# Performance work log

Hardware: AMD Instinct MI355X
Metric: run time of the kernel (lower is better)

The kernel has to match this reference:

```python
import jax, jax.numpy as jnp
import numpy as np

N_HEADS = 16
HEAD_DIM = 128
EPS = 1e-6


def _rmsnorm(t, w):
    # RMSNorm over last dim (head_dim)
    var = jnp.mean(jnp.square(t), axis=-1, keepdims=True)
    return t * jax.lax.rsqrt(var + EPS) * w


def _apply_rope(t, freqs):
    # t: [b, s, h, d]; freqs: [s, 1, d//2, 2, 2]
    b, s, h, d = t.shape
    t2 = t.reshape(b, s, h, 2, d // 2)
    t_ = jnp.moveaxis(t2, -2, -1)[..., None, :].astype(jnp.float32)  # [b,s,h,d/2,1,2]
    out = freqs[..., 0] * t_[..., 0] + freqs[..., 1] * t_[..., 1]    # [b,s,h,d/2,2]
    out = jnp.moveaxis(out, -1, -2).reshape(b, s, h, d)
    return out.astype(t.dtype)


def setup_inputs() -> dict:
    key = jax.random.key(0)
    ks = jax.random.split(key, 8)
    B, S, D = 2, 2048, 2048
    inner = N_HEADS * HEAD_DIM
    sc = 1.0 / np.sqrt(D)
    return {
        "x": jax.random.normal(ks[0], (B, S, D), jnp.float32),
        "rope_emb": jax.random.normal(ks[1], (S, 1, HEAD_DIM // 2, 2, 2), jnp.float32),
        "Wq": jax.random.normal(ks[2], (inner, D), jnp.float32) * sc,
        "Wk": jax.random.normal(ks[3], (inner, D), jnp.float32) * sc,
        "Wv": jax.random.normal(ks[4], (inner, D), jnp.float32) * sc,
        "Wo": jax.random.normal(ks[5], (D, inner), jnp.float32) * sc,
        "q_norm_w": jnp.ones((HEAD_DIM,), jnp.float32),
        "k_norm_w": jnp.ones((HEAD_DIM,), jnp.float32),
    }


def reference(x, rope_emb, Wq, Wk, Wv, Wo, q_norm_w, k_norm_w):
    b, s, _ = x.shape
    h, d = N_HEADS, HEAD_DIM
    q = (x @ Wq.T).reshape(b, s, h, d)
    k = (x @ Wk.T).reshape(b, s, h, d)
    v = (x @ Wv.T).reshape(b, s, h, d)
    q = _apply_rope(_rmsnorm(q, q_norm_w), rope_emb)
    k = _apply_rope(_rmsnorm(k, k_norm_w), rope_emb)
    # SDPA, heads-first layout
    qh = jnp.transpose(q, (0, 2, 1, 3))  # [b,h,s,d]
    kh = jnp.transpose(k, (0, 2, 1, 3))
    vh = jnp.transpose(v, (0, 2, 1, 3))
    scale = 1.0 / np.sqrt(d)
    scores = jnp.einsum('bhqd,bhkd->bhqk', qh, kh) * scale
    attn = jax.nn.softmax(scores, axis=-1)
    out = jnp.einsum('bhqk,bhkd->bhqd', attn, vh)  # [b,h,s,d]
    out = jnp.transpose(out, (0, 2, 1, 3)).reshape(b, s, h * d)
    return out @ Wo.T
```

## Files before the change

### kernel.cpp

```cpp
#include <hip/hip_runtime.h>
#include <hip/hip_bf16.h>
#include <stdint.h>

typedef __bf16 bf16;
typedef __bf16 bf16x4 __attribute__((ext_vector_type(4)));
typedef __bf16 bf16x8 __attribute__((ext_vector_type(8)));
typedef float f32x4 __attribute__((ext_vector_type(4)));
typedef float f32x16 __attribute__((ext_vector_type(16)));

#define N_HEADS 16
#define HEAD_DIM 128
#define SEQ 2048
#define DIM 2048
#define BATCH 2
#define MROWS (BATCH * SEQ)
#define NQKV (3 * DIM)
#define SM_SCALE 0.08838834764831845f
#define SMAX 24.0f

__device__ __forceinline__ bf16 f2b(float f) {
  union { __hip_bfloat16 h; bf16 b; } u;
  u.h = __float2bfloat16(f);
  return u.b;
}

__device__ __forceinline__ void async16(const bf16* g, bf16* l) {
  __builtin_amdgcn_global_load_lds(
      (__attribute__((address_space(1))) void*)(uintptr_t)g,
      (__attribute__((address_space(3))) void*)(uintptr_t)l,
      16, 0, 0);
}

__global__ __launch_bounds__(256) void cvt_kernel(const float* __restrict__ src,
                                                  bf16* __restrict__ dst, int n) {
  int i = (blockIdx.x * 256 + threadIdx.x) * 8;
  if (i >= n) return;
  float4 a = *(const float4*)(src + i);
  float4 b = *(const float4*)(src + i + 4);
  bf16x8 o;
  o[0] = f2b(a.x); o[1] = f2b(a.y); o[2] = f2b(a.z); o[3] = f2b(a.w);
  o[4] = f2b(b.x); o[5] = f2b(b.y); o[6] = f2b(b.z); o[7] = f2b(b.w);
  *(bf16x8*)(dst + i) = o;
}

__device__ __forceinline__ void gemm_tile_mainloop(
    const bf16* __restrict__ A, const bf16* __restrict__ Bw, int K,
    int rowBase, int colBase, bf16* lA, bf16* lB, f32x4 acc[4][4]) {
  const int t = threadIdx.x;
  const int w = t >> 6, lane = t & 63;
  const int lm = lane & 15, quad = lane >> 4;
  const int wr = (w >> 1) * 64, wc = (w & 1) * 64;

  for (int kt = 0; kt < K; kt += 32) {
#pragma unroll
    for (int i = 0; i < 2; i++) {
      const int c = i * 256 + t;
      const int r = c >> 2, cc = (c & 3) << 3;
      async16(A + (size_t)(rowBase + r) * K + (kt + cc), lA + (i * 256 + w * 64) * 8);
      async16(Bw + (size_t)(colBase + r) * K + (kt + cc), lB + (i * 256 + w * 64) * 8);
    }
    asm volatile("s_waitcnt vmcnt(0)" ::: "memory");
    __syncthreads();
    bf16x8 af[4], bfr[4];
#pragma unroll
    for (int f = 0; f < 4; f++)
      af[f] = *(const bf16x8*)(lA + (wr + f * 16 + lm) * 32 + quad * 8);
#pragma unroll
    for (int f = 0; f < 4; f++)
      bfr[f] = *(const bf16x8*)(lB + (wc + f * 16 + lm) * 32 + quad * 8);
#pragma unroll
    for (int fr = 0; fr < 4; fr++)
#pragma unroll
      for (int fc = 0; fc < 4; fc++)
        acc[fr][fc] = __builtin_amdgcn_mfma_f32_16x16x32_bf16(af[fr], bfr[fc], acc[fr][fc], 0, 0, 0);
    __syncthreads();
  }
}

__global__ __launch_bounds__(256) void gemm_qkv(const bf16* __restrict__ X,
                                                const bf16* __restrict__ W,
                                                bf16* __restrict__ Q,
                                                bf16* __restrict__ Kv,
                                                bf16* __restrict__ VT) {
  __shared__ __align__(16) bf16 lA[128 * 32];
  __shared__ __align__(16) bf16 lB[128 * 32];
  f32x4 acc[4][4];
  f32x4 z = {0.f, 0.f, 0.f, 0.f};
#pragma unroll
  for (int i = 0; i < 4; i++)
#pragma unroll
    for (int j = 0; j < 4; j++) acc[i][j] = z;

  const int rowBase = blockIdx.y * 128, colBase = blockIdx.x * 128;
  gemm_tile_mainloop(X, W, DIM, rowBase, colBase, lA, lB, acc);

  const int t = threadIdx.x, w = t >> 6, lane = t & 63;
  const int lm = lane & 15, quad = lane >> 4;
  const int wr = (w >> 1) * 64, wc = (w & 1) * 64;
  const int which = colBase >> 11;
  if (which < 2) {
    bf16* dst = which ? Kv : Q;
#pragma unroll
    for (int fr = 0; fr < 4; fr++)
#pragma unroll
      for (int fc = 0; fc < 4; fc++)
#pragma unroll
        for (int r = 0; r < 4; r++) {
          int m = rowBase + wr + fr * 16 + quad * 4 + r;
          int n = (colBase + wc + fc * 16 + lm) & 2047;
          int h = n >> 7, d = n & 127;
          int b = m >> 11, s = m & 2047;
          dst[(((size_t)(b * N_HEADS + h) * SEQ) + s) * HEAD_DIM + d] = f2b(acc[fr][fc][r]);
        }
  } else {
#pragma unroll
    for (int fr = 0; fr < 4; fr++)
#pragma unroll
      for (int fc = 0; fc < 4; fc++) {
        int n = (colBase + wc + fc * 16 + lm) & 2047;
        int h = n >> 7, d = n & 127;
        int m = rowBase + wr + fr * 16 + quad * 4;
        int b = m >> 11, s = m & 2047;
        bf16x4 pk;
#pragma unroll
        for (int r = 0; r < 4; r++) pk[r] = f2b(acc[fr][fc][r]);
        *(bf16x4*)&VT[((size_t)(b * N_HEADS + h) * HEAD_DIM + d) * SEQ + s] = pk;
      }
  }
}

__global__ __launch_bounds__(256) void gemm_out(const bf16* __restrict__ A,
                                                const bf16* __restrict__ W,
                                                float* __restrict__ out) {
  __shared__ __align__(16) bf16 lA[128 * 32];
  __shared__ __align__(16) bf16 lB[128 * 32];
  f32x4 acc[4][4];
  f32x4 z = {0.f, 0.f, 0.f, 0.f};
#pragma unroll
  for (int i = 0; i < 4; i++)
#pragma unroll
    for (int j = 0; j < 4; j++) acc[i][j] = z;

  const int rowBase = blockIdx.y * 128, colBase = blockIdx.x * 128;
  gemm_tile_mainloop(A, W, DIM, rowBase, colBase, lA, lB, acc);

  const int t = threadIdx.x, w = t >> 6, lane = t & 63;
  const int lm = lane & 15, quad = lane >> 4;
  const int wr = (w >> 1) * 64, wc = (w & 1) * 64;
#pragma unroll
  for (int fr = 0; fr < 4; fr++)
#pragma unroll
    for (int fc = 0; fc < 4; fc++)
#pragma unroll
      for (int r = 0; r < 4; r++) {
        int m = rowBase + wr + fr * 16 + quad * 4 + r;
        int n = colBase + wc + fc * 16 + lm;
        out[(size_t)m * DIM + n] = acc[fr][fc][r];
      }
}

__global__ __launch_bounds__(256) void norm_rope(bf16* __restrict__ Q,
                                                 bf16* __restrict__ K,
                                                 const float* __restrict__ rope,
                                                 const float* __restrict__ qw,
                                                 const float* __restrict__ kw) {
  const int t = threadIdx.x, w = t >> 6, lane = t & 63;
  const int rid = blockIdx.x * 4 + w;
  const int which = rid >> 16;
  const int row = rid & 65535;
  bf16* ptr = (which ? K : Q) + (size_t)row * HEAD_DIM;
  const float* nw = which ? kw : qw;
  const int s = row & (SEQ - 1);

  float x0 = (float)ptr[lane];
  float x1 = (float)ptr[lane + 64];
  float ss = x0 * x0 + x1 * x1;
#pragma unroll
  for (int off = 32; off; off >>= 1) ss += __shfl_xor(ss, off);
  float r = rsqrtf(ss * (1.f / 128.f) + 1e-6f);
  float x0n = x0 * r * nw[lane];
  float x1n = x1 * r * nw[lane + 64];
  float4 f = ((const float4*)rope)[s * 64 + lane];
  float y0 = f.x * x0n + f.y * x1n;
  float y1 = f.z * x0n + f.w * x1n;
  if (!which) { y0 *= SM_SCALE; y1 *= SM_SCALE; }
  ptr[lane] = f2b(y0);
  ptr[lane + 64] = f2b(y1);
}

__global__ __launch_bounds__(256, 3) void attn_kernel(const bf16* __restrict__ Q,
                                                      const bf16* __restrict__ K,
                                                      const bf16* __restrict__ VT,
                                                      bf16* __restrict__ O) {
  __shared__ __align__(16) bf16 Ks[64 * 128];
  __shared__ __align__(16) bf16 Vs[128 * 64];
  __shared__ __align__(16) bf16 Ps[4][32][72];

  const int t = threadIdx.x, w = t >> 6, lane = t & 63;
  const int l31 = lane & 31, half = lane >> 5;
  const int qt = blockIdx.x, bh = blockIdx.y;

  const bf16* Qp = Q + ((size_t)bh * SEQ + qt * 128 + w * 32 + l31) * HEAD_DIM;
  bf16x8 qf[8];
#pragma unroll
  for (int ks = 0; ks < 8; ks++)
    qf[ks] = *(const bf16x8*)(Qp + ks * 16 + half * 8);

  f32x16 oacc[4];
#pragma unroll
  for (int nb = 0; nb < 4; nb++)
#pragma unroll
    for (int e = 0; e < 16; e++) oacc[nb][e] = 0.f;
  float rsum = 0.f;

  const bf16* kbase = K + (size_t)bh * SEQ * HEAD_DIM;
  const bf16* vbase = VT + (size_t)bh * HEAD_DIM * SEQ;

  for (int j = 0; j < SEQ / 64; j++) {
    const bf16* kp = kbase + (size_t)j * 64 * HEAD_DIM;
    const bf16* vp = vbase + j * 64;
#pragma unroll
    for (int i = 0; i < 4; i++) {
      int c = i * 256 + t;
      int kr = c >> 4, cc = c & 15;
      bf16x8 tmp = *(const bf16x8*)(kp + kr * 128 + cc * 8);
      *(bf16x8*)&Ks[kr * 128 + ((cc ^ (kr & 15)) << 3)] = tmp;
    }
#pragma unroll
    for (int i = 0; i < 4; i++) {
      int c = i * 256 + t;
      int d = c >> 3, cc = c & 7;
      bf16x8 tmp = *(const bf16x8*)(vp + (size_t)d * SEQ + cc * 8);
      *(bf16x8*)&Vs[d * 64 + ((cc ^ (d & 7)) << 3)] = tmp;
    }
    __syncthreads();

#pragma unroll
    for (int mb = 0; mb < 2; mb++) {
      f32x16 sacc;
#pragma unroll
      for (int e = 0; e < 16; e++) sacc[e] = -SMAX;
      const int kr = mb * 32 + l31;
#pragma unroll
      for (int ks = 0; ks < 8; ks++) {
        int c = ks * 2 + half;
        bf16x8 kf = *(const bf16x8*)&Ks[kr * 128 + ((c ^ (kr & 15)) << 3)];
        sacc = __builtin_amdgcn_mfma_f32_32x32x16_bf16(kf, qf[ks], sacc, 0, 0, 0);
      }
#pragma unroll
      for (int g = 0; g < 4; g++) {
        bf16x4 pk;
#pragma unroll
        for (int e = 0; e < 4; e++) {
          float p = __expf(sacc[g * 4 + e]);
          rsum += p;
          pk[e] = f2b(p);
        }
        *(bf16x4*)&Ps[w][l31][mb * 32 + g * 8 + half * 4] = pk;
      }
    }

#pragma unroll
    for (int ks2 = 0; ks2 < 4; ks2++) {
      bf16x8 ap = *(const bf16x8*)&Ps[w][l31][ks2 * 16 + half * 8];
      int c = ks2 * 2 + half;
#pragma unroll
      for (int nb = 0; nb < 4; nb++) {
        int rv = nb * 32 + l31;
        bf16x8 bv = *(const bf16x8*)&Vs[rv * 64 + ((c ^ (rv & 7)) << 3)];
        oacc[nb] = __builtin_amdgcn_mfma_f32_32x32x16_bf16(ap, bv, oacc[nb], 0, 0, 0);
      }
    }
    __syncthreads();
  }

  rsum += __shfl_xor(rsum, 32);
  float inv = 1.f / rsum;
  const int b = bh >> 4, h = bh & 15;
#pragma unroll
  for (int r = 0; r < 16; r++) {
    int row = (r & 3) + 8 * (r >> 2) + 4 * half;
    float iv = __shfl(inv, row);
    int qg = qt * 128 + w * 32 + row;
    size_t orow = ((size_t)b * SEQ + qg) * DIM + h * HEAD_DIM + l31;
#pragma unroll
    for (int nb = 0; nb < 4; nb++)
      O[orow + nb * 32] = f2b(oacc[nb][r] * iv);
  }
}

extern "C" void kernel_launch(void* const* d_in, const int* in_sizes, int n_in,
                              void* d_out, int out_size, void* d_ws, size_t ws_size,
                              hipStream_t stream) {
  const float* x    = (const float*)d_in[0];
  const float* rope = (const float*)d_in[1];
  const float* Wq   = (const float*)d_in[2];
  const float* Wk   = (const float*)d_in[3];
  const float* Wv   = (const float*)d_in[4];
  const float* Wo   = (const float*)d_in[5];
  const float* qw   = (const float*)d_in[6];
  const float* kw   = (const float*)d_in[7];
  float* out = (float*)d_out;

  char* ws = (char*)d_ws;
  bf16* xb   = (bf16*)ws;
  bf16* wqkv = (bf16*)(ws + (16u << 20));
  bf16* wo   = (bf16*)(ws + (40u << 20));
  bf16* qb   = (bf16*)(ws + (48u << 20));
  bf16* kb   = (bf16*)(ws + (64u << 20));
  bf16* vt   = (bf16*)(ws + (80u << 20));
  bf16* attn = xb;

  const int NX = MROWS * DIM;
  const int NW = DIM * DIM;

  cvt_kernel<<<NX / 8 / 256, 256, 0, stream>>>(x, xb, NX);
  cvt_kernel<<<NW / 8 / 256, 256, 0, stream>>>(Wq, wqkv, NW);
  cvt_kernel<<<NW / 8 / 256, 256, 0, stream>>>(Wk, wqkv + NW, NW);
  cvt_kernel<<<NW / 8 / 256, 256, 0, stream>>>(Wv, wqkv + 2 * (size_t)NW, NW);
  cvt_kernel<<<NW / 8 / 256, 256, 0, stream>>>(Wo, wo, NW);

  gemm_qkv<<<dim3(NQKV / 128, MROWS / 128), 256, 0, stream>>>(xb, wqkv, qb, kb, vt);
  norm_rope<<<(2 * BATCH * N_HEADS * SEQ) / 4, 256, 0, stream>>>(qb, kb, rope, qw, kw);
  attn_kernel<<<dim3(SEQ / 128, BATCH * N_HEADS), 256, 0, stream>>>(qb, kb, vt, attn);
  gemm_out<<<dim3(DIM / 128, MROWS / 128), 256, 0, stream>>>(attn, wo, out);
}
```

Baseline: 466.6 us.

## Split attention waves over key halves with 64-row query tiles and async LDS loads

Each wave now handles 64 query rows against one 32-key half of each 64-key tile, so every K fragment read from LDS feeds two MFMAs. The partial outputs and row sums from the two key halves are combined through shared memory at the end. K and V tiles are loaded with direct global-to-LDS async copies instead of going through registers. The change doubles the accumulator registers, so launch bounds drop to two blocks per SM, and it adds an LDS reduction epilogue with extra barriers.

```diff
diff --git a/kernel.cpp b/kernel.cpp
--- a/kernel.cpp
+++ b/kernel.cpp
@@ -188,33 +188,41 @@
   ptr[lane + 64] = f2b(y1);
 }
 
-__global__ __launch_bounds__(256, 3) void attn_kernel(const bf16* __restrict__ Q,
+__global__ __launch_bounds__(256, 2) void attn_kernel(const bf16* __restrict__ Q,
                                                       const bf16* __restrict__ K,
                                                       const bf16* __restrict__ VT,
                                                       bf16* __restrict__ O) {
   __shared__ __align__(16) bf16 Ks[64 * 128];
   __shared__ __align__(16) bf16 Vs[128 * 64];
-  __shared__ __align__(16) bf16 Ps[4][32][72];
+  __shared__ __align__(16) bf16 Ps[4][64 * 36];
 
   const int t = threadIdx.x, w = t >> 6, lane = t & 63;
-  const int l31 = lane & 31, half = lane >> 5;
+  const int lq = lane & 31, h = lane >> 5;
+  const int qh = w >> 1, kb = w & 1;
   const int qt = blockIdx.x, bh = blockIdx.y;
 
-  const bf16* Qp = Q + ((size_t)bh * SEQ + qt * 128 + w * 32 + l31) * HEAD_DIM;
-  bf16x8 qf[8];
-#pragma unroll
-  for (int ks = 0; ks < 8; ks++)
-    qf[ks] = *(const bf16x8*)(Qp + ks * 16 + half * 8);
-
-  f32x16 oacc[4];
-#pragma unroll
-  for (int nb = 0; nb < 4; nb++)
-#pragma unroll
-    for (int e = 0; e < 16; e++) oacc[nb][e] = 0.f;
-  float rsum = 0.f;
+  bf16x8 qf[2][8];
+#pragma unroll
+  for (int qs = 0; qs < 2; qs++) {
+    const bf16* Qp = Q + ((size_t)bh * SEQ + qt * 128 + qh * 64 + qs * 32 + lq) * HEAD_DIM;
+#pragma unroll
+    for (int ks = 0; ks < 8; ks++)
+      qf[qs][ks] = *(const bf16x8*)(Qp + ks * 16 + h * 8);
+  }
+
+  f32x16 oacc[2][4];
+#pragma unroll
+  for (int qs = 0; qs < 2; qs++)
+#pragma unroll
+    for (int nb = 0; nb < 4; nb++)
+#pragma unroll
+      for (int e = 0; e < 16; e++) oacc[qs][nb][e] = 0.f;
+  float rsum[2] = {0.f, 0.f};
 
   const bf16* kbase = K + (size_t)bh * SEQ * HEAD_DIM;
   const bf16* vbase = VT + (size_t)bh * HEAD_DIM * SEQ;
+  bf16* myPs = Ps[w];
+  const int kr = kb * 32 + lq;
 
   for (int j = 0; j < SEQ / 64; j++) {
     const bf16* kp = kbase + (size_t)j * 64 * HEAD_DIM;
@@ -222,70 +230,102 @@
 #pragma unroll
     for (int i = 0; i < 4; i++) {
       int c = i * 256 + t;
-      int kr = c >> 4, cc = c & 15;
-      bf16x8 tmp = *(const bf16x8*)(kp + kr * 128 + cc * 8);
-      *(bf16x8*)&Ks[kr * 128 + ((cc ^ (kr & 15)) << 3)] = tmp;
+      int r = c >> 4, cc = c & 15;
+      async16(kp + r * 128 + (((cc ^ (r & 15)) & 15) << 3), Ks + (i * 256 + w * 64) * 8);
     }
 #pragma unroll
     for (int i = 0; i < 4; i++) {
       int c = i * 256 + t;
       int d = c >> 3, cc = c & 7;
-      bf16x8 tmp = *(const bf16x8*)(vp + (size_t)d * SEQ + cc * 8);
-      *(bf16x8*)&Vs[d * 64 + ((cc ^ (d & 7)) << 3)] = tmp;
-    }
-    __syncthreads();
-
-#pragma unroll
-    for (int mb = 0; mb < 2; mb++) {
-      f32x16 sacc;
-#pragma unroll
-      for (int e = 0; e < 16; e++) sacc[e] = -SMAX;
-      const int kr = mb * 32 + l31;
-#pragma unroll
-      for (int ks = 0; ks < 8; ks++) {
-        int c = ks * 2 + half;
-        bf16x8 kf = *(const bf16x8*)&Ks[kr * 128 + ((c ^ (kr & 15)) << 3)];
-        sacc = __builtin_amdgcn_mfma_f32_32x32x16_bf16(kf, qf[ks], sacc, 0, 0, 0);
-      }
+      async16(vp + (size_t)d * SEQ + (((cc ^ (d & 7)) & 7) << 3), Vs + (i * 256 + w * 64) * 8);
+    }
+    asm volatile("s_waitcnt vmcnt(0)" ::: "memory");
+    __syncthreads();
+
+    f32x16 sacc[2];
+#pragma unroll
+    for (int qs = 0; qs < 2; qs++)
+#pragma unroll
+      for (int e = 0; e < 16; e++) sacc[qs][e] = -SMAX;
+#pragma unroll
+    for (int ks = 0; ks < 8; ks++) {
+      int c = ks * 2 + h;
+      bf16x8 kf = *(const bf16x8*)&Ks[kr * 128 + ((c ^ (kr & 15)) << 3)];
+      sacc[0] = __builtin_amdgcn_mfma_f32_32x32x16_bf16(kf, qf[0][ks], sacc[0], 0, 0, 0);
+      sacc[1] = __builtin_amdgcn_mfma_f32_32x32x16_bf16(kf, qf[1][ks], sacc[1], 0, 0, 0);
+    }
+
+#pragma unroll
+    for (int qs = 0; qs < 2; qs++)
 #pragma unroll
       for (int g = 0; g < 4; g++) {
         bf16x4 pk;
 #pragma unroll
         for (int e = 0; e < 4; e++) {
-          float p = __expf(sacc[g * 4 + e]);
-          rsum += p;
+          float p = __expf(sacc[qs][g * 4 + e]);
+          rsum[qs] += p;
           pk[e] = f2b(p);
         }
-        *(bf16x4*)&Ps[w][l31][mb * 32 + g * 8 + half * 4] = pk;
-      }
-    }
-
-#pragma unroll
-    for (int ks2 = 0; ks2 < 4; ks2++) {
-      bf16x8 ap = *(const bf16x8*)&Ps[w][l31][ks2 * 16 + half * 8];
-      int c = ks2 * 2 + half;
+        *(bf16x4*)&myPs[(qs * 32 + lq) * 36 + g * 8 + h * 4] = pk;
+      }
+
+#pragma unroll
+    for (int ks2 = 0; ks2 < 2; ks2++) {
+      bf16x8 ap0 = *(const bf16x8*)&myPs[lq * 36 + ks2 * 16 + h * 8];
+      bf16x8 ap1 = *(const bf16x8*)&myPs[(32 + lq) * 36 + ks2 * 16 + h * 8];
+      int c2 = kb * 4 + ks2 * 2 + h;
 #pragma unroll
       for (int nb = 0; nb < 4; nb++) {
-        int rv = nb * 32 + l31;
-        bf16x8 bv = *(const bf16x8*)&Vs[rv * 64 + ((c ^ (rv & 7)) << 3)];
-        oacc[nb] = __builtin_amdgcn_mfma_f32_32x32x16_bf16(ap, bv, oacc[nb], 0, 0, 0);
-      }
-    }
-    __syncthreads();
-  }
-
-  rsum += __shfl_xor(rsum, 32);
-  float inv = 1.f / rsum;
-  const int b = bh >> 4, h = bh & 15;
-#pragma unroll
-  for (int r = 0; r < 16; r++) {
-    int row = (r & 3) + 8 * (r >> 2) + 4 * half;
-    float iv = __shfl(inv, row);
-    int qg = qt * 128 + w * 32 + row;
-    size_t orow = ((size_t)b * SEQ + qg) * DIM + h * HEAD_DIM + l31;
-#pragma unroll
-    for (int nb = 0; nb < 4; nb++)
-      O[orow + nb * 32] = f2b(oacc[nb][r] * iv);
+        int rv = nb * 32 + lq;
+        bf16x8 bv = *(const bf16x8*)&Vs[rv * 64 + ((c2 ^ (rv & 7)) << 3)];
+        oacc[0][nb] = __builtin_amdgcn_mfma_f32_32x32x16_bf16(ap0, bv, oacc[0][nb], 0, 0, 0);
+        oacc[1][nb] = __builtin_amdgcn_mfma_f32_32x32x16_bf16(ap1, bv, oacc[1][nb], 0, 0, 0);
+      }
+    }
+    __syncthreads();
+  }
+
+  rsum[0] += __shfl_xor(rsum[0], 32);
+  rsum[1] += __shfl_xor(rsum[1], 32);
+  float* Om = (float*)Ks;
+  float* Rs = (float*)Vs;
+  const int pair = qh;
+  const int b = bh >> 4, hh = bh & 15;
+  float inv[2] = {0.f, 0.f};
+
+#pragma unroll
+  for (int nb = 0; nb < 4; nb++) {
+    if (kb == 1) {
+      if (nb == 0 && h == 0) {
+        Rs[(pair * 2 + 0) * 32 + lq] = rsum[0];
+        Rs[(pair * 2 + 1) * 32 + lq] = rsum[1];
+      }
+#pragma unroll
+      for (int qs = 0; qs < 2; qs++)
+#pragma unroll
+        for (int r = 0; r < 16; r++) {
+          int rowm = (r & 3) + 8 * (r >> 2) + 4 * h;
+          Om[(pair * 64 + qs * 32 + rowm) * 32 + lq] = oacc[qs][nb][r];
+        }
+    }
+    __syncthreads();
+    if (kb == 0) {
+      if (nb == 0) {
+        inv[0] = 1.f / (rsum[0] + Rs[(pair * 2 + 0) * 32 + lq]);
+        inv[1] = 1.f / (rsum[1] + Rs[(pair * 2 + 1) * 32 + lq]);
+      }
+#pragma unroll
+      for (int qs = 0; qs < 2; qs++)
+#pragma unroll
+        for (int r = 0; r < 16; r++) {
+          int rowm = (r & 3) + 8 * (r >> 2) + 4 * h;
+          float val = oacc[qs][nb][r] + Om[(pair * 64 + qs * 32 + rowm) * 32 + lq];
+          float iv = __shfl(inv[qs], rowm);
+          int qg = qt * 128 + qh * 64 + qs * 32 + rowm;
+          O[((size_t)b * SEQ + qg) * DIM + hh * HEAD_DIM + nb * 32 + lq] = f2b(val * iv);
+        }
+    }
+    __syncthreads();
   }
 }
 
```

Result: slower. 578.5 us (+24.0%).
